# Kernel optimization log

Hardware: AMD Instinct MI355X
Metric: run time of the kernel (lower is better)

The kernel has to match this reference:

```python
import jax, jax.numpy as jnp
import numpy as np

B = 8192
HID = [256, 128, 64]
OUT = 5
EPS = 1e-5

# neighbor order for branch i: all other branches in ascending index order
NEIGH = np.array([[j for j in range(8) if j != i] for i in range(8)])  # [8,7]
# adjacency gate (row,col) into A.view(-1,8,8) for branch i, neighbor slot k
# (branch 1 uses a transposed pattern for slots 3..6, exactly as in the source)
_G = [
    [(0,1),(0,2),(0,3),(4,0),(5,0),(6,0),(7,0)],
    [(0,1),(2,1),(3,1),(4,1),(5,1),(6,1),(7,1)],
    [(0,2),(1,2),(3,2),(4,2),(5,2),(6,2),(7,2)],
    [(0,3),(1,3),(2,3),(4,3),(5,3),(6,3),(7,3)],
    [(0,4),(1,4),(2,4),(3,4),(5,4),(6,4),(7,4)],
    [(0,5),(1,5),(2,5),(3,5),(4,5),(6,5),(7,5)],
    [(0,6),(1,6),(2,6),(3,6),(4,6),(5,6),(7,6)],
    [(0,7),(1,7),(2,7),(3,7),(4,7),(5,7),(6,7)],
]
GIDX = np.array([[r * 8 + c for (r, c) in row] for row in _G]).reshape(-1)  # [56]


def setup_inputs() -> dict:
    key = jax.random.key(0)
    ks = iter(jax.random.split(key, 64))
    inp = {}
    inp["state"] = jax.random.normal(next(ks), (B, 3), jnp.float32)
    for i in range(1, 9):
        inp[f"Z{i}"] = jax.random.normal(next(ks), (B, 3), jnp.float32)
    inp["A"] = jax.random.uniform(next(ks), (B, 64), jnp.float32)
    din = 3
    for l, dout in enumerate(HID):
        inp[f"W{l}"] = jax.random.normal(next(ks), (8, din, dout), jnp.float32) * 0.05
        inp[f"b{l}"] = jnp.zeros((8, dout), jnp.float32)
        inp[f"g{l}"] = jnp.ones((8, dout), jnp.float32)
        inp[f"be{l}"] = jnp.zeros((8, dout), jnp.float32)
        inp[f"Wg{l}"] = jax.random.normal(next(ks), (8, 7 * din, 7), jnp.float32) * 0.05
        inp[f"bg{l}"] = jnp.zeros((8, 7), jnp.float32)
        din = dout
    inp["Wout"] = jax.random.normal(next(ks), (8, din, OUT), jnp.float32) * 0.05
    inp["bout"] = jnp.zeros((8, OUT), jnp.float32)
    return inp


def _forward(Z, A, layers, Wout, bout):
    # Z: [B,8,D0], A: [B,64]
    b = Z.shape[0]
    gates = A[:, jnp.asarray(GIDX)].reshape(b, 8, 7)  # [B,8,7]
    neigh = jnp.asarray(NEIGH)
    for (W, bias, g, be, Wg, bg) in layers:
        Zn = Z[:, neigh, :]                                   # [B,8,7,D]
        Zall = Zn.reshape(b, 8, -1)                           # [B,8,7D]
        a = jax.nn.softmax(jnp.einsum('bif,ifo->bio', Zall, Wg) + bg, axis=-1)
        NZ = jnp.einsum('bik,bikd->bid', a * gates, Zn)       # attention-weighted neighbor sum
        h = jnp.einsum('bid,ido->bio', Z + NZ, W) + bias
        mu = h.mean(-1, keepdims=True)
        var = ((h - mu) ** 2).mean(-1, keepdims=True)
        h = (h - mu) / jnp.sqrt(var + EPS) * g + be           # per-branch LayerNorm
        Z = jax.nn.relu(h)
    return jnp.tanh(jnp.einsum('bid,ido->bio', Z, Wout) + bout)  # [B,8,5]


def reference(state, Z1, Z2, Z3, Z4, Z5, Z6, Z7, Z8, A,
              W0, b0, g0, be0, Wg0, bg0,
              W1, b1, g1, be1, Wg1, bg1,
              W2, b2, g2, be2, Wg2, bg2,
              Wout, bout):
    Z = jnp.stack([Z1, Z2, Z3, Z4, Z5, Z6, Z7, Z8], axis=1)  # [B,8,3]
    layers = [(W0, b0, g0, be0, Wg0, bg0),
              (W1, b1, g1, be1, Wg1, bg1),
              (W2, b2, g2, be2, Wg2, bg2)]
    return _forward(Z, A, layers, Wout, bout)
```

## Files before the change

### kernel.cpp

```cpp
#include <hip/hip_runtime.h>
#include <math.h>

typedef _Float16 v8h __attribute__((ext_vector_type(8)));
typedef float    v4f __attribute__((ext_vector_type(4)));

#define NB    32
#define DSTR  264
#define WSTR  68
#define EPSLN 1e-5f

struct KP {
  const float* Z[8];
  const float* A;
  const float *W0, *b0, *g0, *be0, *Wg0, *bg0;
  const float *b1, *g1, *be1, *bg1;
  const float *b2, *g2, *be2, *bg2;
  const float *bout;
  const _Float16 *WgT1, *WgT2, *WT1, *WT2, *WoT;
  float* out;
};

__device__ __forceinline__ void cvt_one(const float* __restrict__ src, _Float16* __restrict__ dst,
                                        int F, int Osrc, int Opad, int t) {
  const int f  = t % F;
  const int io = t / F;
  const int o  = io % Opad;
  const int i  = io / Opad;
  dst[t] = (o < Osrc) ? (_Float16)src[(i * F + f) * Osrc + o] : (_Float16)0.f;
}

#define E1 114688
#define E2 57344
#define E3 4096
#define E4 262144
#define E5 65536

__global__ void cvt_all(const float* __restrict__ Wg1, const float* __restrict__ Wg2,
                        const float* __restrict__ Wout, const float* __restrict__ W1,
                        const float* __restrict__ W2, _Float16* __restrict__ ws) {
  int t = blockIdx.x * 256 + threadIdx.x;
  if (t < E1) { cvt_one(Wg1, ws, 1792, 7, 8, t); return; }
  t -= E1;
  if (t < E2) { cvt_one(Wg2, ws + E1, 896, 7, 8, t); return; }
  t -= E2;
  if (t < E3) { cvt_one(Wout, ws + E1 + E2, 64, 5, 8, t); return; }
  t -= E3;
  if (t < E4) { cvt_one(W1, ws + E1 + E2 + E3, 256, 128, 128, t); return; }
  t -= E4;
  if (t < E5) { cvt_one(W2, ws + E1 + E2 + E3 + E4, 128, 64, 64, t); return; }
}

template<int D, int O>
__device__ __forceinline__ void mfma_layer(
    _Float16* __restrict__ zh, float* __restrict__ wbuf, const float* __restrict__ gbuf,
    const _Float16* __restrict__ WgT, const float* __restrict__ bg,
    const _Float16* __restrict__ WT, const float* __restrict__ bias,
    const float* __restrict__ g, const float* __restrict__ be,
    int i, int q, int r)
{
  constexpr int KS = D / 32;
  constexpr int NT = O / 16;

  const _Float16* WgB = WgT + (size_t)(i * 8 + r) * (7 * D) + q * 8;
  const _Float16* WB  = WT  + (size_t)(i * O + r) * D + q * 8;

  v8h gbf[7], dbf[NT];
  #pragma unroll
  for (int nb = 0; nb < 7; ++nb) gbf[nb] = *(const v8h*)(WgB + nb * D);
  #pragma unroll
  for (int n = 0; n < NT; ++n)  dbf[n]  = *(const v8h*)(WB + (size_t)n * 16 * D);

  v4f gacc0 = (v4f){0.f,0.f,0.f,0.f}, gacc1 = (v4f){0.f,0.f,0.f,0.f};
  #pragma unroll
  for (int ks = 0; ks < KS; ++ks) {
    const int d0 = ks * 32 + q * 8;
    v8h gbn[7];
    if (ks + 1 < KS) {
      #pragma unroll
      for (int nb = 0; nb < 7; ++nb)
        gbn[nb] = *(const v8h*)(WgB + nb * D + (ks + 1) * 32);
    }
    #pragma unroll
    for (int nb = 0; nb < 7; ++nb) {
      const int nk = nb + (nb >= i);
      const v8h af0 = *(const v8h*)(zh + (nk * NB + r) * DSTR + d0);
      const v8h af1 = *(const v8h*)(zh + (nk * NB + 16 + r) * DSTR + d0);
      gacc0 = __builtin_amdgcn_mfma_f32_16x16x32_f16(af0, gbf[nb], gacc0, 0, 0, 0);
      gacc1 = __builtin_amdgcn_mfma_f32_16x16x32_f16(af1, gbf[nb], gacc1, 0, 0, 0);
    }
    if (ks + 1 < KS) {
      #pragma unroll
      for (int nb = 0; nb < 7; ++nb) gbf[nb] = gbn[nb];
    }
  }
  const float bgv = (r < 7) ? bg[i * 7 + r] : 0.f;
  #pragma unroll
  for (int mt = 0; mt < 2; ++mt) {
    const v4f ga = mt ? gacc1 : gacc0;
    #pragma unroll
    for (int reg = 0; reg < 4; ++reg) {
      const float v = ga[reg] + bgv;
      float m = (r < 7) ? v : -3.0e38f;
      #pragma unroll
      for (int mk = 1; mk < 16; mk <<= 1) m = fmaxf(m, __shfl_xor(m, mk, 16));
      const float e = (r < 7) ? __expf(v - m) : 0.f;
      float s = e;
      #pragma unroll
      for (int mk = 1; mk < 16; mk <<= 1) s += __shfl_xor(s, mk, 16);
      const int b = mt * 16 + q * 4 + reg;
      if (r < 7) wbuf[b * WSTR + i * 8 + r] = (e / s) * gbuf[b * WSTR + i * 8 + r];
    }
  }
  __syncthreads();

  v4f acc[2][NT];
  #pragma unroll
  for (int mt = 0; mt < 2; ++mt)
    #pragma unroll
    for (int n = 0; n < NT; ++n) acc[mt][n] = (v4f){0.f,0.f,0.f,0.f};

  _Float16 wh[2][7];
  #pragma unroll
  for (int mt = 0; mt < 2; ++mt)
    #pragma unroll
    for (int nb = 0; nb < 7; ++nb)
      wh[mt][nb] = (_Float16)wbuf[(mt * 16 + r) * WSTR + i * 8 + nb];

  #pragma unroll
  for (int ks = 0; ks < KS; ++ks) {
    const int d0 = ks * 32 + q * 8;
    v8h dbn[NT];
    if (ks + 1 < KS) {
      #pragma unroll
      for (int n = 0; n < NT; ++n)
        dbn[n] = *(const v8h*)(WB + (size_t)n * 16 * D + (ks + 1) * 32);
    }
    v8h x01[2];
    #pragma unroll
    for (int mt = 0; mt < 2; ++mt) {
      v8h zn[7];
      #pragma unroll
      for (int nb = 0; nb < 7; ++nb) {
        const int nk = nb + (nb >= i);
        zn[nb] = *(const v8h*)(zh + ((nk * NB + mt * 16 + r) * DSTR + d0));
      }
      v8h x = *(const v8h*)(zh + ((i * NB + mt * 16 + r) * DSTR + d0));
      x = (x + (zn[0] * wh[mt][0] + zn[1] * wh[mt][1]))
        + ((zn[2] * wh[mt][2] + zn[3] * wh[mt][3])
        + ((zn[4] * wh[mt][4] + zn[5] * wh[mt][5]) + zn[6] * wh[mt][6]));
      x01[mt] = x;
    }
    #pragma unroll
    for (int n = 0; n < NT; ++n) {
      acc[0][n] = __builtin_amdgcn_mfma_f32_16x16x32_f16(x01[0], dbf[n], acc[0][n], 0, 0, 0);
      acc[1][n] = __builtin_amdgcn_mfma_f32_16x16x32_f16(x01[1], dbf[n], acc[1][n], 0, 0, 0);
    }
    if (ks + 1 < KS) {
      #pragma unroll
      for (int n = 0; n < NT; ++n) dbf[n] = dbn[n];
    }
  }

  float bv[NT], gv[NT], bev[NT];
  #pragma unroll
  for (int n = 0; n < NT; ++n) {
    const int o = n * 16 + r;
    bv[n] = bias[i * O + o]; gv[n] = g[i * O + o]; bev[n] = be[i * O + o];
  }
  #pragma unroll
  for (int mt = 0; mt < 2; ++mt) {
    #pragma unroll
    for (int reg = 0; reg < 4; ++reg) {
      float s1 = 0.f, s2 = 0.f;
      #pragma unroll
      for (int n = 0; n < NT; ++n) {
        const float h = acc[mt][n][reg] + bv[n];
        acc[mt][n][reg] = h;
        s1 += h; s2 += h * h;
      }
      #pragma unroll
      for (int mk = 1; mk < 16; mk <<= 1) { s1 += __shfl_xor(s1, mk, 16); s2 += __shfl_xor(s2, mk, 16); }
      const float mean = s1 * (1.f / O);
      const float var  = s2 * (1.f / O) - mean * mean;
      const float rs   = rsqrtf(var + EPSLN);
      #pragma unroll
      for (int n = 0; n < NT; ++n) {
        const float h = (acc[mt][n][reg] - mean) * rs * gv[n] + bev[n];
        acc[mt][n][reg] = fmaxf(h, 0.f);
      }
    }
  }
  __syncthreads();
  #pragma unroll
  for (int mt = 0; mt < 2; ++mt)
    #pragma unroll
    for (int n = 0; n < NT; ++n)
      #pragma unroll
      for (int reg = 0; reg < 4; ++reg) {
        const int b = mt * 16 + q * 4 + reg;
        zh[(i * NB + b) * DSTR + n * 16 + r] = (_Float16)acc[mt][n][reg];
      }
  __syncthreads();
}

__launch_bounds__(512, 2)
__global__ void actor_mfma(KP p)
{
  __shared__ __align__(16) _Float16 zh[8 * NB * DSTR];
  __shared__ float wbuf[NB * WSTR];
  __shared__ float gbuf[NB * WSTR];
  __shared__ float xbuf[8 * NB * 4];

  const int i = threadIdx.x >> 6;
  const int u = threadIdx.x & 63;
  const int q = u >> 4, r = u & 15;
  const int bbase = blockIdx.x * NB;

  {
    #pragma unroll
    for (int c = 0; c < 2; ++c) {
      const int idx = c * 64 + u;
      if (idx < NB * 3) {
        const int b = idx / 3, d = idx - 3 * (idx / 3);
        zh[(i * NB + b) * DSTR + d] = (_Float16)p.Z[i][(size_t)(bbase + b) * 3 + d];
      }
    }
    for (int t = threadIdx.x; t < NB * 64; t += 512) {
      const int b = t >> 6, ik = t & 63;
      const int ii = ik >> 3, k = ik & 7;
      if (k < 7) {
        const int j = k + (k >= ii);
        const int gidx = (ii == 0 && j <= 3) ? j : 8 * j + ii;
        gbuf[b * WSTR + ik] = p.A[(size_t)(bbase + b) * 64 + gidx];
      }
    }
  }
  __syncthreads();

  for (int c = 0; c < NB / 8; ++c) {
    const int b = c * 8 + (u >> 3), o8 = u & 7;
    float v = -3.0e38f;
    if (o8 < 7) {
      v = p.bg0[i * 7 + o8];
      #pragma unroll
      for (int k = 0; k < 7; ++k) {
        const int nk = k + (k >= i);
        const _Float16* zp = zh + (nk * NB + b) * DSTR;
        const float* wp = p.Wg0 + (i * 21 + k * 3) * 7 + o8;
        v += (float)zp[0] * wp[0] + (float)zp[1] * wp[7] + (float)zp[2] * wp[14];
      }
    }
    float m = v;
    #pragma unroll
    for (int mk = 1; mk < 8; mk <<= 1) m = fmaxf(m, __shfl_xor(m, mk, 8));
    const float e = (o8 < 7) ? __expf(v - m) : 0.f;
    float s = e;
    #pragma unroll
    for (int mk = 1; mk < 8; mk <<= 1) s += __shfl_xor(s, mk, 8);
    if (o8 < 7) wbuf[b * WSTR + i * 8 + o8] = (e / s) * gbuf[b * WSTR + i * 8 + o8];
  }
  __syncthreads();
  #pragma unroll
  for (int c = 0; c < 2; ++c) {
    const int idx = c * 64 + u;
    if (idx < NB * 3) {
      const int b = idx / 3, d = idx - 3 * (idx / 3);
      float x = (float)zh[(i * NB + b) * DSTR + d];
      #pragma unroll
      for (int k = 0; k < 7; ++k) {
        const int nk = k + (k >= i);
        x += wbuf[b * WSTR + i * 8 + k] * (float)zh[(nk * NB + b) * DSTR + d];
      }
      xbuf[(i * NB + b) * 4 + d] = x;
    }
  }
  __syncthreads();
  {
    const int bh = u >> 5, lo = u & 31, o = lo * 8;
    float w0r[3][8], b0r[8], g0r[8], be0r[8];
    #pragma unroll
    for (int d = 0; d < 3; ++d)
      #pragma unroll
      for (int j = 0; j < 8; ++j) w0r[d][j] = p.W0[(i * 3 + d) * 256 + o + j];
    #pragma unroll
    for (int j = 0; j < 8; ++j) {
      b0r[j] = p.b0[i * 256 + o + j];
      g0r[j] = p.g0[i * 256 + o + j];
      be0r[j] = p.be0[i * 256 + o + j];
    }
    for (int it = 0; it < NB / 2; ++it) {
      const int b = it * 2 + bh;
      const float x0 = xbuf[(i * NB + b) * 4 + 0];
      const float x1 = xbuf[(i * NB + b) * 4 + 1];
      const float x2 = xbuf[(i * NB + b) * 4 + 2];
      float h[8], s1 = 0.f, s2 = 0.f;
      #pragma unroll
      for (int j = 0; j < 8; ++j) {
        const float v = b0r[j] + x0 * w0r[0][j] + x1 * w0r[1][j] + x2 * w0r[2][j];
        h[j] = v; s1 += v; s2 += v * v;
      }
      #pragma unroll
      for (int mk = 1; mk < 32; mk <<= 1) { s1 += __shfl_xor(s1, mk, 32); s2 += __shfl_xor(s2, mk, 32); }
      const float mean = s1 * (1.f / 256.f);
      const float var  = s2 * (1.f / 256.f) - mean * mean;
      const float rs   = rsqrtf(var + EPSLN);
      v8h hv;
      #pragma unroll
      for (int j = 0; j < 8; ++j)
        hv[j] = (_Float16)fmaxf((h[j] - mean) * rs * g0r[j] + be0r[j], 0.f);
      *(v8h*)(zh + (i * NB + b) * DSTR + o) = hv;
    }
  }
  __syncthreads();

  mfma_layer<256, 128>(zh, wbuf, gbuf, p.WgT1, p.bg1, p.WT1, p.b1, p.g1, p.be1, i, q, r);
  mfma_layer<128, 64 >(zh, wbuf, gbuf, p.WgT2, p.bg2, p.WT2, p.b2, p.g2, p.be2, i, q, r);

  {
    const int b8 = u >> 3, o8 = u & 7;
    v8h wreg[8];
    #pragma unroll
    for (int t8 = 0; t8 < 8; ++t8)
      wreg[t8] = *(const v8h*)(p.WoT + (i * 8 + o8) * 64 + t8 * 8);
    const float bo = (o8 < 5) ? p.bout[i * 5 + o8] : 0.f;
    for (int c = 0; c < NB / 8; ++c) {
      const int b = c * 8 + b8;
      const _Float16* zp = zh + (i * NB + b) * DSTR;
      float acc = bo;
      #pragma unroll
      for (int t8 = 0; t8 < 8; ++t8) {
        const v8h z8 = *(const v8h*)(zp + t8 * 8);
        #pragma unroll
        for (int j = 0; j < 8; ++j) acc += (float)z8[j] * (float)wreg[t8][j];
      }
      if (o8 < 5)
        p.out[((size_t)(bbase + b) * 8 + i) * 5 + o8] = tanhf(acc);
    }
  }
}

extern "C" void kernel_launch(void* const* d_in, const int* in_sizes, int n_in,
                              void* d_out, int out_size, void* d_ws, size_t ws_size,
                              hipStream_t stream) {
  KP p;
  for (int i = 0; i < 8; ++i) p.Z[i] = (const float*)d_in[1 + i];
  p.A   = (const float*)d_in[9];
  p.W0  = (const float*)d_in[10]; p.b0 = (const float*)d_in[11];
  p.g0  = (const float*)d_in[12]; p.be0 = (const float*)d_in[13];
  p.Wg0 = (const float*)d_in[14]; p.bg0 = (const float*)d_in[15];
  const float* W1  = (const float*)d_in[16]; p.b1 = (const float*)d_in[17];
  p.g1  = (const float*)d_in[18]; p.be1 = (const float*)d_in[19];
  const float* Wg1 = (const float*)d_in[20]; p.bg1 = (const float*)d_in[21];
  const float* W2  = (const float*)d_in[22]; p.b2 = (const float*)d_in[23];
  p.g2  = (const float*)d_in[24]; p.be2 = (const float*)d_in[25];
  const float* Wg2 = (const float*)d_in[26]; p.bg2 = (const float*)d_in[27];
  const float* Wout = (const float*)d_in[28]; p.bout = (const float*)d_in[29];
  p.out = (float*)d_out;

  _Float16* wsH = (_Float16*)d_ws;
  p.WgT1 = wsH;
  p.WgT2 = wsH + E1;
  p.WoT  = wsH + E1 + E2;
  p.WT1  = wsH + E1 + E2 + E3;
  p.WT2  = wsH + E1 + E2 + E3 + E4;

  const int total = E1 + E2 + E3 + E4 + E5;
  hipLaunchKernelGGL(cvt_all, dim3((total + 255) / 256), dim3(256), 0, stream,
                     Wg1, Wg2, Wout, W1, W2, wsH);

  hipLaunchKernelGGL(actor_mfma, dim3(8192 / NB), dim3(512), 0, stream, p);
}
```

Baseline: 78.52 us.

## Prefetch next-layer weights across layers, split gate MFMA chains, drop wave-local syncs

```diff
diff --git a/kernel.cpp b/kernel.cpp
--- a/kernel.cpp
+++ b/kernel.cpp
@@ -50,12 +50,14 @@
   if (t < E5) { cvt_one(W2, ws + E1 + E2 + E3 + E4, 128, 64, 64, t); return; }
 }
 
-template<int D, int O>
+template<int D, int O, int NPRE>
 __device__ __forceinline__ void mfma_layer(
     _Float16* __restrict__ zh, float* __restrict__ wbuf, const float* __restrict__ gbuf,
+    const v8h* gpre,
     const _Float16* __restrict__ WgT, const float* __restrict__ bg,
     const _Float16* __restrict__ WT, const float* __restrict__ bias,
     const float* __restrict__ g, const float* __restrict__ be,
+    const _Float16* __restrict__ preBase, int preStride, v8h* pre,
     int i, int q, int r)
 {
   constexpr int KS = D / 32;
@@ -64,13 +66,20 @@
   const _Float16* WgB = WgT + (size_t)(i * 8 + r) * (7 * D) + q * 8;
   const _Float16* WB  = WT  + (size_t)(i * O + r) * D + q * 8;
 
-  v8h gbf[7], dbf[NT];
-  #pragma unroll
-  for (int nb = 0; nb < 7; ++nb) gbf[nb] = *(const v8h*)(WgB + nb * D);
-  #pragma unroll
-  for (int n = 0; n < NT; ++n)  dbf[n]  = *(const v8h*)(WB + (size_t)n * 16 * D);
-
-  v4f gacc0 = (v4f){0.f,0.f,0.f,0.f}, gacc1 = (v4f){0.f,0.f,0.f,0.f};
+  v8h dbf[NT];
+  #pragma unroll
+  for (int n = 0; n < NT; ++n) dbf[n] = *(const v8h*)(WB + (size_t)n * 16 * D);
+
+  v8h gbf[7];
+  #pragma unroll
+  for (int nb = 0; nb < 7; ++nb) gbf[nb] = gpre[nb];
+
+  v4f ca[2][2];
+  #pragma unroll
+  for (int mt = 0; mt < 2; ++mt)
+    #pragma unroll
+    for (int c = 0; c < 2; ++c) ca[mt][c] = (v4f){0.f,0.f,0.f,0.f};
+
   #pragma unroll
   for (int ks = 0; ks < KS; ++ks) {
     const int d0 = ks * 32 + q * 8;
@@ -85,21 +94,22 @@
       const int nk = nb + (nb >= i);
       const v8h af0 = *(const v8h*)(zh + (nk * NB + r) * DSTR + d0);
       const v8h af1 = *(const v8h*)(zh + (nk * NB + 16 + r) * DSTR + d0);
-      gacc0 = __builtin_amdgcn_mfma_f32_16x16x32_f16(af0, gbf[nb], gacc0, 0, 0, 0);
-      gacc1 = __builtin_amdgcn_mfma_f32_16x16x32_f16(af1, gbf[nb], gacc1, 0, 0, 0);
+      ca[0][nb & 1] = __builtin_amdgcn_mfma_f32_16x16x32_f16(af0, gbf[nb], ca[0][nb & 1], 0, 0, 0);
+      ca[1][nb & 1] = __builtin_amdgcn_mfma_f32_16x16x32_f16(af1, gbf[nb], ca[1][nb & 1], 0, 0, 0);
     }
     if (ks + 1 < KS) {
       #pragma unroll
       for (int nb = 0; nb < 7; ++nb) gbf[nb] = gbn[nb];
     }
   }
+  const v4f gacc[2] = { ca[0][0] + ca[0][1], ca[1][0] + ca[1][1] };
+
   const float bgv = (r < 7) ? bg[i * 7 + r] : 0.f;
   #pragma unroll
   for (int mt = 0; mt < 2; ++mt) {
-    const v4f ga = mt ? gacc1 : gacc0;
     #pragma unroll
     for (int reg = 0; reg < 4; ++reg) {
-      const float v = ga[reg] + bgv;
+      const float v = gacc[mt][reg] + bgv;
       float m = (r < 7) ? v : -3.0e38f;
       #pragma unroll
       for (int mk = 1; mk < 16; mk <<= 1) m = fmaxf(m, __shfl_xor(m, mk, 16));
@@ -111,7 +121,6 @@
       if (r < 7) wbuf[b * WSTR + i * 8 + r] = (e / s) * gbuf[b * WSTR + i * 8 + r];
     }
   }
-  __syncthreads();
 
   v4f acc[2][NT];
   #pragma unroll
@@ -160,6 +169,10 @@
       for (int n = 0; n < NT; ++n) dbf[n] = dbn[n];
     }
   }
+
+  #pragma unroll
+  for (int t = 0; t < NPRE; ++t)
+    pre[t] = *(const v8h*)(preBase + (size_t)t * preStride);
 
   float bv[NT], gv[NT], bev[NT];
   #pragma unroll
@@ -259,7 +272,6 @@
     for (int mk = 1; mk < 8; mk <<= 1) s += __shfl_xor(s, mk, 8);
     if (o8 < 7) wbuf[b * WSTR + i * 8 + o8] = (e / s) * gbuf[b * WSTR + i * 8 + o8];
   }
-  __syncthreads();
   #pragma unroll
   for (int c = 0; c < 2; ++c) {
     const int idx = c * 64 + u;
@@ -273,6 +285,12 @@
       }
       xbuf[(i * NB + b) * 4 + d] = x;
     }
+  }
+  v8h gpre1[7];
+  {
+    const _Float16* gb = p.WgT1 + (size_t)(i * 8 + r) * (7 * 256) + q * 8;
+    #pragma unroll
+    for (int nb = 0; nb < 7; ++nb) gpre1[nb] = *(const v8h*)(gb + nb * 256);
   }
   __syncthreads();
   {
@@ -313,15 +331,14 @@
   }
   __syncthreads();
 
-  mfma_layer<256, 128>(zh, wbuf, gbuf, p.WgT1, p.bg1, p.WT1, p.b1, p.g1, p.be1, i, q, r);
-  mfma_layer<128, 64 >(zh, wbuf, gbuf, p.WgT2, p.bg2, p.WT2, p.b2, p.g2, p.be2, i, q, r);
+  v8h gpre2[7], wpre[8];
+  mfma_layer<256, 128, 7>(zh, wbuf, gbuf, gpre1, p.WgT1, p.bg1, p.WT1, p.b1, p.g1, p.be1,
+                          p.WgT2 + (size_t)(i * 8 + r) * (7 * 128) + q * 8, 128, gpre2, i, q, r);
+  mfma_layer<128, 64, 8>(zh, wbuf, gbuf, gpre2, p.WgT2, p.bg2, p.WT2, p.b2, p.g2, p.be2,
+                         p.WoT + (size_t)(i * 8 + (u & 7)) * 64, 8, wpre, i, q, r);
 
   {
     const int b8 = u >> 3, o8 = u & 7;
-    v8h wreg[8];
-    #pragma unroll
-    for (int t8 = 0; t8 < 8; ++t8)
-      wreg[t8] = *(const v8h*)(p.WoT + (i * 8 + o8) * 64 + t8 * 8);
     const float bo = (o8 < 5) ? p.bout[i * 5 + o8] : 0.f;
     for (int c = 0; c < NB / 8; ++c) {
       const int b = c * 8 + b8;
@@ -331,7 +348,7 @@
       for (int t8 = 0; t8 < 8; ++t8) {
         const v8h z8 = *(const v8h*)(zp + t8 * 8);
         #pragma unroll
-        for (int j = 0; j < 8; ++j) acc += (float)z8[j] * (float)wreg[t8][j];
+        for (int j = 0; j < 8; ++j) acc += (float)z8[j] * (float)wpre[t8][j];
       }
       if (o8 < 5)
         p.out[((size_t)(bbase + b) * 8 + i) * 5 + o8] = tanhf(acc);
```

Result: faster. 75.70 us (-3.6%).
